# Performance work log

Hardware: AMD Instinct MI355X
Metric: run time of the kernel (lower is better)

## Reference

```python
import jax, jax.numpy as jnp
import numpy as np

B, L, D, H, S, V, K = 2, 64, 1024, 512, 50000, 40000, 32
SLM_LOGITS_SCALE = 0.1
BN_EPS = 1e-5


def setup_inputs() -> dict:
    key = jax.random.key(0)
    ks = jax.random.split(key, 8)
    return {
        "cached_embeddings": jax.random.normal(ks[0], (B, L, D), dtype=jnp.float32),
        "bn_gamma": jnp.ones((L,), jnp.float32),
        "bn_beta": jnp.zeros((L,), jnp.float32),
        "W1": jax.random.normal(ks[1], (D, H), dtype=jnp.float32) * 0.02,
        "b1": jnp.zeros((H,), jnp.float32),
        "W2": jax.random.normal(ks[2], (H, S), dtype=jnp.float32) * 0.02,
        "b2": jnp.zeros((S,), jnp.float32),
        "W_slm": jax.random.normal(ks[3], (H, V), dtype=jnp.float32) * 0.02,
        "b_slm": jnp.zeros((V,), jnp.float32),
        # fixed degree k=32 with values 1/min(deg,k) = 1/32 (full-degree rows)
        "sl_weights": jnp.full((S, K), 1.0 / K, jnp.float32),
        "sl_idx": jax.random.randint(ks[4], (S, K), 0, V, dtype=jnp.int32),
    }


def reference(cached_embeddings, bn_gamma, bn_beta, W1, b1, W2, b2,
              W_slm, b_slm, sl_weights, sl_idx):
    x = cached_embeddings  # [B, L, D]
    # BatchNorm1d(win_size): channels are sequence positions; stats over (B, D)
    mean = jnp.mean(x, axis=(0, 2), keepdims=True)
    var = jnp.var(x, axis=(0, 2), keepdims=True)
    xn = (x - mean) * jax.lax.rsqrt(var + BN_EPS)
    x = xn * bn_gamma[None, :, None] + bn_beta[None, :, None]
    # DenseEncoder: hidden + sense logits
    h = jax.nn.relu(jnp.einsum('bld,dh->blh', x, W1) + b1)  # [B, L, H]
    y = jnp.einsum('blh,hs->bls', h, W2) + b2                # [B, L, S]
    # SLM head: lemma logits
    v = jnp.einsum('blh,hv->blv', h, W_slm) + b_slm          # [B, L, V]
    # sparse sense->lemma matmul == weighted bounded-degree gather-sum
    g = v[..., sl_idx]                                       # [B, L, S, K]
    slm_logits = jnp.einsum('blsk,sk->bls', g, sl_weights)   # [B, L, S]
    return y + slm_logits * SLM_LOGITS_SCALE
```

## Files before the change

### kernel.cpp

```cpp
#include <hip/hip_runtime.h>
#include <hip/hip_fp8.h>

#define LL 64
#define DD 1024
#define HH 512
#define SS 50000
#define VV 40000
#define KD 32
#define MM 128

typedef __bf16 bf16_t;
typedef __bf16 bf16x8 __attribute__((ext_vector_type(8)));
typedef __bf16 bf16x4 __attribute__((ext_vector_type(4)));
typedef __bf16 bf16x2 __attribute__((ext_vector_type(2)));
typedef float f32x4 __attribute__((ext_vector_type(4)));

__device__ __forceinline__ void async_ld16(const void* g, void* l) {
    __builtin_amdgcn_global_load_lds(
        (const __attribute__((address_space(1))) void*)g,
        (__attribute__((address_space(3))) void*)l, 16, 0, 0);
}

__global__ __launch_bounds__(256) void k_bn(const float* __restrict__ x,
        const float* __restrict__ gamma, const float* __restrict__ beta,
        bf16_t* __restrict__ xn) {
    int l = blockIdx.x;
    int t = threadIdx.x;
    int b = t >> 7;
    int d0 = (t & 127) << 3;
    const float* xp = x + (size_t)(b * LL + l) * DD + d0;
    float4 v0 = *(const float4*)xp;
    float4 v1 = *(const float4*)(xp + 4);
    float s  = v0.x + v0.y + v0.z + v0.w + v1.x + v1.y + v1.z + v1.w;
    float ss = v0.x*v0.x + v0.y*v0.y + v0.z*v0.z + v0.w*v0.w
             + v1.x*v1.x + v1.y*v1.y + v1.z*v1.z + v1.w*v1.w;
    #pragma unroll
    for (int off = 32; off > 0; off >>= 1) {
        s  += __shfl_xor(s, off);
        ss += __shfl_xor(ss, off);
    }
    __shared__ float red[8];
    int wv = t >> 6, ln = t & 63;
    if (ln == 0) { red[wv] = s; red[4 + wv] = ss; }
    __syncthreads();
    float tot  = red[0] + red[1] + red[2] + red[3];
    float tots = red[4] + red[5] + red[6] + red[7];
    float mean = tot * (1.0f / 2048.0f);
    float var  = tots * (1.0f / 2048.0f) - mean * mean;
    float rstd = rsqrtf(var + 1e-5f);
    float g   = gamma[l] * rstd;
    float ofs = beta[l] - mean * g;
    bf16x8 o;
    o[0] = (bf16_t)(v0.x * g + ofs);
    o[1] = (bf16_t)(v0.y * g + ofs);
    o[2] = (bf16_t)(v0.z * g + ofs);
    o[3] = (bf16_t)(v0.w * g + ofs);
    o[4] = (bf16_t)(v1.x * g + ofs);
    o[5] = (bf16_t)(v1.y * g + ofs);
    o[6] = (bf16_t)(v1.z * g + ofs);
    o[7] = (bf16_t)(v1.w * g + ofs);
    *(bf16x8*)(xn + (size_t)(b * LL + l) * DD + d0) = o;
}

__global__ __launch_bounds__(128) void k_gemm1(const bf16_t* __restrict__ xn,
        const float* __restrict__ W1, const float* __restrict__ b1,
        bf16_t* __restrict__ h) {
    int t = threadIdx.x;
    int wv = t >> 6, lane = t & 63;
    int c = lane & 15, q = lane >> 4;
    int tile = blockIdx.x;
    int tm = tile >> 5, tn = tile & 31;
    int col = tn * 16 + c;
    f32x4 acc = {};
    for (int kk = wv * 512; kk < wv * 512 + 512; kk += 32) {
        bf16x8 afr = *(const bf16x8*)(xn + (size_t)(tm * 16 + c) * DD + kk + q * 8);
        bf16x8 bfr;
        #pragma unroll
        for (int j = 0; j < 8; ++j)
            bfr[j] = (bf16_t)W1[(size_t)(kk + q * 8 + j) * HH + col];
        acc = __builtin_amdgcn_mfma_f32_16x16x32_bf16(afr, bfr, acc, 0, 0, 0);
    }
    __shared__ float red[64 * 4];
    if (wv == 1) {
        #pragma unroll
        for (int r = 0; r < 4; ++r) red[lane * 4 + r] = acc[r];
    }
    __syncthreads();
    if (wv == 0) {
        float bias = b1[col];
        #pragma unroll
        for (int r = 0; r < 4; ++r) {
            int m = tm * 16 + q * 4 + r;
            float v = acc[r] + red[lane * 4 + r] + bias;
            h[(size_t)m * HH + col] = (bf16_t)(v > 0.f ? v : 0.f);
        }
    }
}

__global__ __launch_bounds__(256) void k_gemm_v(const bf16_t* __restrict__ h,
        const float* __restrict__ Wslm, const float* __restrict__ bslm,
        unsigned char* __restrict__ vT8) {
    __shared__ float wt[2][64 * 64];
    int t = threadIdx.x;
    int wv = t >> 6, lane = t & 63;
    int c = lane & 15, q = lane >> 4;
    int nb = blockIdx.x * 64;
    int col = nb + wv * 16 + c;
    int r  = t >> 4, sg = t & 15;
    int phase = (blockIdx.x * 5) & 7;
    const float* gbase = Wslm + (size_t)r * VV + nb + sg * 4;

    #define STAGE_V(buf, kk) do { \
        _Pragma("unroll") \
        for (int i = 0; i < 4; ++i) \
            async_ld16(gbase + (size_t)((kk) + 16 * i) * VV, \
                       &wt[buf][t * 4 + i * 1024]); } while (0)

    STAGE_V(0, phase * 64);
    f32x4 acc[8] = {};
    #pragma unroll 1
    for (int step = 0; step < 8; ++step) {
        int cur = step & 1;
        __syncthreads();
        if (step < 7) STAGE_V(cur ^ 1, (((step + 1 + phase) & 7) * 64));
        int kk = ((step + phase) & 7) * 64;
        #pragma unroll
        for (int kh = 0; kh < 2; ++kh) {
            bf16x8 bfr;
            #pragma unroll
            for (int j = 0; j < 8; ++j)
                bfr[j] = (bf16_t)wt[cur][(kh * 32 + q * 8 + j) * 64 + wv * 16 + c];
            #pragma unroll
            for (int ms = 0; ms < 8; ++ms) {
                bf16x8 afr = *(const bf16x8*)(h + (size_t)(ms * 16 + c) * HH
                                              + kk + kh * 32 + q * 8);
                acc[ms] = __builtin_amdgcn_mfma_f32_16x16x32_bf16(afr, bfr, acc[ms], 0, 0, 0);
            }
        }
    }
    float bias = bslm[col];
    #pragma unroll
    for (int ms = 0; ms < 8; ++ms) {
        union { unsigned int u; unsigned char b[4]; } pk;
        #pragma unroll
        for (int rr = 0; rr < 4; ++rr) {
            __hip_fp8_e4m3 f8(acc[ms][rr] + bias);
            pk.b[rr] = f8.__x;
        }
        *(unsigned int*)(vT8 + (size_t)col * MM + ms * 16 + q * 4) = pk.u;
    }
    #undef STAGE_V
}

__global__ __launch_bounds__(256) void k_gather(const unsigned char* __restrict__ vT8,
        const float* __restrict__ slw, const int* __restrict__ slidx,
        bf16_t* __restrict__ slm) {
    int t = threadIdx.x;
    int wv = t >> 6, lane = t & 63;
    int s = blockIdx.x * 4 + wv;
    int idv = slidx[(size_t)s * KD + (lane & 31)];
    float wgt = slw[(size_t)s * KD + (lane & 31)];
    unsigned short u[KD];
    #pragma unroll
    for (int k = 0; k < KD; ++k) {
        int id = __shfl(idv, k);
        u[k] = *(const unsigned short*)(vT8 + (size_t)id * MM + lane * 2);
    }
    float a0 = 0.f, a1 = 0.f;
    #pragma unroll
    for (int k = 0; k < KD; ++k) {
        float w = __shfl(wgt, k);
        __hip_fp8_e4m3 f0, f1;
        f0.__x = (unsigned char)(u[k] & 0xff);
        f1.__x = (unsigned char)(u[k] >> 8);
        a0 += w * (float)f0;
        a1 += w * (float)f1;
    }
    bf16x2 o;
    o[0] = (bf16_t)a0;
    o[1] = (bf16_t)a1;
    *(bf16x2*)(slm + (size_t)s * MM + lane * 2) = o;
}

__global__ __launch_bounds__(256) void k_gemm_y(const bf16_t* __restrict__ h,
        const float* __restrict__ W2, const float* __restrict__ b2,
        const bf16_t* __restrict__ slm, float* __restrict__ out) {
    __shared__ float wt[2][64 * 64];
    int t = threadIdx.x;
    int wv = t >> 6, lane = t & 63;
    int c = lane & 15, q = lane >> 4;
    int nb = blockIdx.x * 64;
    int col = nb + wv * 16 + c;
    int r  = t >> 4, sg = t & 15;
    int sgc = nb + sg * 4;
    bool ok = (sgc + 4 <= SS);
    const float* gbase = ok ? (W2 + (size_t)r * SS + sgc) : W2;
    int phase = (blockIdx.x * 5) & 7;

    #define STAGE_Y(buf, kk) do { \
        _Pragma("unroll") \
        for (int i = 0; i < 4; ++i) \
            async_ld16(gbase + (size_t)((kk) + 16 * i) * SS, \
                       &wt[buf][t * 4 + i * 1024]); } while (0)

    STAGE_Y(0, phase * 64);
    f32x4 acc[8] = {};
    #pragma unroll 1
    for (int step = 0; step < 8; ++step) {
        int cur = step & 1;
        __syncthreads();
        if (step < 7) STAGE_Y(cur ^ 1, (((step + 1 + phase) & 7) * 64));
        int kk = ((step + phase) & 7) * 64;
        #pragma unroll
        for (int kh = 0; kh < 2; ++kh) {
            bf16x8 bfr;
            #pragma unroll
            for (int j = 0; j < 8; ++j)
                bfr[j] = (bf16_t)wt[cur][(kh * 32 + q * 8 + j) * 64 + wv * 16 + c];
            #pragma unroll
            for (int ms = 0; ms < 8; ++ms) {
                bf16x8 afr = *(const bf16x8*)(h + (size_t)(ms * 16 + c) * HH
                                              + kk + kh * 32 + q * 8);
                acc[ms] = __builtin_amdgcn_mfma_f32_16x16x32_bf16(afr, bfr, acc[ms], 0, 0, 0);
            }
        }
    }
    if (col < SS) {
        float bias = b2[col];
        #pragma unroll
        for (int ms = 0; ms < 8; ++ms) {
            bf16x4 sv = *(const bf16x4*)(slm + (size_t)col * MM + ms * 16 + q * 4);
            #pragma unroll
            for (int rr = 0; rr < 4; ++rr) {
                int m = ms * 16 + q * 4 + rr;
                out[(size_t)m * SS + col] = acc[ms][rr] + bias + 0.1f * (float)sv[rr];
            }
        }
    }
    #undef STAGE_Y
}

extern "C" void kernel_launch(void* const* d_in, const int* in_sizes, int n_in,
                              void* d_out, int out_size, void* d_ws, size_t ws_size,
                              hipStream_t stream) {
    const float* x     = (const float*)d_in[0];
    const float* gamma = (const float*)d_in[1];
    const float* beta  = (const float*)d_in[2];
    const float* W1    = (const float*)d_in[3];
    const float* b1    = (const float*)d_in[4];
    const float* W2    = (const float*)d_in[5];
    const float* b2    = (const float*)d_in[6];
    const float* Wslm  = (const float*)d_in[7];
    const float* bslm  = (const float*)d_in[8];
    const float* slw   = (const float*)d_in[9];
    const int*   slidx = (const int*)d_in[10];
    float* out = (float*)d_out;

    char* ws = (char*)d_ws;
    bf16_t*        xn  = (bf16_t*)ws;
    bf16_t*        h   = (bf16_t*)(ws + 262144);
    unsigned char* vT8 = (unsigned char*)(ws + 393216);
    bf16_t*        slm = (bf16_t*)(ws + 5513216);

    k_bn    <<<64,    256, 0, stream>>>(x, gamma, beta, xn);
    k_gemm1 <<<256,   128, 0, stream>>>(xn, W1, b1, h);
    k_gemm_v<<<625,   256, 0, stream>>>(h, Wslm, bslm, vT8);
    k_gather<<<12500, 256, 0, stream>>>(vT8, slw, slidx, slm);
    k_gemm_y<<<782,   256, 0, stream>>>(h, W2, b2, slm, out);
}
```

Before: 364.9 us.

## Load GEMM weights directly into registers with triple-buffered prefetch, dropping LDS staging

Both weight-streaming GEMM kernels (SLM head and sense head) stop staging fp32 weight tiles through LDS with async global-to-LDS loads and barriers. Each lane now loads its own 8 weight values per 32-wide k-step straight into registers, prefetching two steps ahead in a 3-deep register ring, and uses launch bounds of 3 blocks per SM. This removes LDS traffic, __syncthreads and the per-element LDS reads when building B fragments. In exchange it uses more registers, loses the per-block phase offset over k, and issues strided scalar loads that stay coalesced only across the 16 adjacent columns in a row.

```diff
diff --git a/kernel.cpp b/kernel.cpp
--- a/kernel.cpp
+++ b/kernel.cpp
@@ -14,12 +14,6 @@
 typedef __bf16 bf16x4 __attribute__((ext_vector_type(4)));
 typedef __bf16 bf16x2 __attribute__((ext_vector_type(2)));
 typedef float f32x4 __attribute__((ext_vector_type(4)));
-
-__device__ __forceinline__ void async_ld16(const void* g, void* l) {
-    __builtin_amdgcn_global_load_lds(
-        (const __attribute__((address_space(1))) void*)g,
-        (__attribute__((address_space(3))) void*)l, 16, 0, 0);
-}
 
 __global__ __launch_bounds__(256) void k_bn(const float* __restrict__ x,
         const float* __restrict__ gamma, const float* __restrict__ beta,
@@ -97,45 +91,39 @@
     }
 }
 
-__global__ __launch_bounds__(256) void k_gemm_v(const bf16_t* __restrict__ h,
+__global__ __launch_bounds__(256, 3) void k_gemm_v(const bf16_t* __restrict__ h,
         const float* __restrict__ Wslm, const float* __restrict__ bslm,
         unsigned char* __restrict__ vT8) {
-    __shared__ float wt[2][64 * 64];
     int t = threadIdx.x;
     int wv = t >> 6, lane = t & 63;
     int c = lane & 15, q = lane >> 4;
-    int nb = blockIdx.x * 64;
-    int col = nb + wv * 16 + c;
-    int r  = t >> 4, sg = t & 15;
-    int phase = (blockIdx.x * 5) & 7;
-    const float* gbase = Wslm + (size_t)r * VV + nb + sg * 4;
-
-    #define STAGE_V(buf, kk) do { \
-        _Pragma("unroll") \
-        for (int i = 0; i < 4; ++i) \
-            async_ld16(gbase + (size_t)((kk) + 16 * i) * VV, \
-                       &wt[buf][t * 4 + i * 1024]); } while (0)
-
-    STAGE_V(0, phase * 64);
+    int col = blockIdx.x * 64 + wv * 16 + c;
+    const float* bp = Wslm + (size_t)(q * 8) * VV + col;
+    const bf16_t* ha = h + (size_t)c * HH + q * 8;
+
+    float breg[3][8];
+    #pragma unroll
+    for (int j = 0; j < 8; ++j) breg[0][j] = bp[(size_t)j * VV];
+    #pragma unroll
+    for (int j = 0; j < 8; ++j) breg[1][j] = bp[(size_t)(32 + j) * VV];
+
     f32x4 acc[8] = {};
-    #pragma unroll 1
-    for (int step = 0; step < 8; ++step) {
-        int cur = step & 1;
-        __syncthreads();
-        if (step < 7) STAGE_V(cur ^ 1, (((step + 1 + phase) & 7) * 64));
-        int kk = ((step + phase) & 7) * 64;
-        #pragma unroll
-        for (int kh = 0; kh < 2; ++kh) {
-            bf16x8 bfr;
+    #pragma unroll
+    for (int step = 0; step < 16; ++step) {
+        int kk = step * 32;
+        int cur = step % 3, nxt = (step + 2) % 3;
+        if (step < 14) {
             #pragma unroll
             for (int j = 0; j < 8; ++j)
-                bfr[j] = (bf16_t)wt[cur][(kh * 32 + q * 8 + j) * 64 + wv * 16 + c];
-            #pragma unroll
-            for (int ms = 0; ms < 8; ++ms) {
-                bf16x8 afr = *(const bf16x8*)(h + (size_t)(ms * 16 + c) * HH
-                                              + kk + kh * 32 + q * 8);
-                acc[ms] = __builtin_amdgcn_mfma_f32_16x16x32_bf16(afr, bfr, acc[ms], 0, 0, 0);
-            }
+                breg[nxt][j] = bp[(size_t)(kk + 64 + j) * VV];
+        }
+        bf16x8 bfr;
+        #pragma unroll
+        for (int j = 0; j < 8; ++j) bfr[j] = (bf16_t)breg[cur][j];
+        #pragma unroll
+        for (int ms = 0; ms < 8; ++ms) {
+            bf16x8 afr = *(const bf16x8*)(ha + (size_t)(ms * 16) * HH + kk);
+            acc[ms] = __builtin_amdgcn_mfma_f32_16x16x32_bf16(afr, bfr, acc[ms], 0, 0, 0);
         }
     }
     float bias = bslm[col];
@@ -149,7 +137,6 @@
         }
         *(unsigned int*)(vT8 + (size_t)col * MM + ms * 16 + q * 4) = pk.u;
     }
-    #undef STAGE_V
 }
 
 __global__ __launch_bounds__(256) void k_gather(const unsigned char* __restrict__ vT8,
@@ -182,47 +169,40 @@
     *(bf16x2*)(slm + (size_t)s * MM + lane * 2) = o;
 }
 
-__global__ __launch_bounds__(256) void k_gemm_y(const bf16_t* __restrict__ h,
+__global__ __launch_bounds__(256, 3) void k_gemm_y(const bf16_t* __restrict__ h,
         const float* __restrict__ W2, const float* __restrict__ b2,
         const bf16_t* __restrict__ slm, float* __restrict__ out) {
-    __shared__ float wt[2][64 * 64];
     int t = threadIdx.x;
     int wv = t >> 6, lane = t & 63;
     int c = lane & 15, q = lane >> 4;
-    int nb = blockIdx.x * 64;
-    int col = nb + wv * 16 + c;
-    int r  = t >> 4, sg = t & 15;
-    int sgc = nb + sg * 4;
-    bool ok = (sgc + 4 <= SS);
-    const float* gbase = ok ? (W2 + (size_t)r * SS + sgc) : W2;
-    int phase = (blockIdx.x * 5) & 7;
-
-    #define STAGE_Y(buf, kk) do { \
-        _Pragma("unroll") \
-        for (int i = 0; i < 4; ++i) \
-            async_ld16(gbase + (size_t)((kk) + 16 * i) * SS, \
-                       &wt[buf][t * 4 + i * 1024]); } while (0)
-
-    STAGE_Y(0, phase * 64);
+    int col = blockIdx.x * 64 + wv * 16 + c;
+    int colc = col < SS ? col : SS - 1;
+    const float* bp = W2 + (size_t)(q * 8) * SS + colc;
+    const bf16_t* ha = h + (size_t)c * HH + q * 8;
+
+    float breg[3][8];
+    #pragma unroll
+    for (int j = 0; j < 8; ++j) breg[0][j] = bp[(size_t)j * SS];
+    #pragma unroll
+    for (int j = 0; j < 8; ++j) breg[1][j] = bp[(size_t)(32 + j) * SS];
+
     f32x4 acc[8] = {};
-    #pragma unroll 1
-    for (int step = 0; step < 8; ++step) {
-        int cur = step & 1;
-        __syncthreads();
-        if (step < 7) STAGE_Y(cur ^ 1, (((step + 1 + phase) & 7) * 64));
-        int kk = ((step + phase) & 7) * 64;
-        #pragma unroll
-        for (int kh = 0; kh < 2; ++kh) {
-            bf16x8 bfr;
+    #pragma unroll
+    for (int step = 0; step < 16; ++step) {
+        int kk = step * 32;
+        int cur = step % 3, nxt = (step + 2) % 3;
+        if (step < 14) {
             #pragma unroll
             for (int j = 0; j < 8; ++j)
-                bfr[j] = (bf16_t)wt[cur][(kh * 32 + q * 8 + j) * 64 + wv * 16 + c];
-            #pragma unroll
-            for (int ms = 0; ms < 8; ++ms) {
-                bf16x8 afr = *(const bf16x8*)(h + (size_t)(ms * 16 + c) * HH
-                                              + kk + kh * 32 + q * 8);
-                acc[ms] = __builtin_amdgcn_mfma_f32_16x16x32_bf16(afr, bfr, acc[ms], 0, 0, 0);
-            }
+                breg[nxt][j] = bp[(size_t)(kk + 64 + j) * SS];
+        }
+        bf16x8 bfr;
+        #pragma unroll
+        for (int j = 0; j < 8; ++j) bfr[j] = (bf16_t)breg[cur][j];
+        #pragma unroll
+        for (int ms = 0; ms < 8; ++ms) {
+            bf16x8 afr = *(const bf16x8*)(ha + (size_t)(ms * 16) * HH + kk);
+            acc[ms] = __builtin_amdgcn_mfma_f32_16x16x32_bf16(afr, bfr, acc[ms], 0, 0, 0);
         }
     }
     if (col < SS) {
@@ -237,7 +217,6 @@
             }
         }
     }
-    #undef STAGE_Y
 }
 
 extern "C" void kernel_launch(void* const* d_in, const int* in_sizes, int n_in,
```

Measured after the change: 366.4 us. No clear change (+0.4%).
